# Performance work log

Measured on AMD Instinct MI355X. Metric: run time of the kernel, lower is better.

Reference implementation:

```python
import jax, jax.numpy as jnp
import numpy as np

T = 64
NBITS_PSUM = 8
NBITS_ACC = 8
K = 2
EPS = 1e-5

def _binarize_ste(x):
    # sign binarization with straight-through estimator (torch code overwrites .data)
    s = jnp.where(x >= 0, 1.0, -1.0).astype(x.dtype)
    return x + jax.lax.stop_gradient(s - x)

def _binary_conv_psum(x, w):
    # x: [N,C,H,W], w: [O,C,3,3]. Binarized 3x3 conv (stride 1, pad 1) computed as
    # chunks of T products along the unrolled reduction dim, each partial sum
    # quantized to NBITS_PSUM bits with step K, final accumulator clipped to NBITS_ACC.
    N, C, H, W = x.shape
    O = w.shape[0]
    xb = _binarize_ste(x)
    wb = _binarize_ste(w)
    patches = jax.lax.conv_general_dilated_patches(
        xb, (3, 3), (1, 1), ((1, 1), (1, 1)),
        dimension_numbers=('NCHW', 'OIHW', 'NCHW'))  # [N, C*9, H, W], channel-major
    R = C * 9
    nch = R // T  # 2304 / 64 = 36 chunks
    p = patches.reshape(N, nch, T, H, W).transpose(1, 0, 2, 3, 4)  # [nch,N,T,H,W]
    wf = wb.reshape(O, nch, T).transpose(1, 0, 2)                   # [nch,O,T]
    qmax = 2 ** (NBITS_PSUM - 1) - 1
    step = float(K)

    def body(carry, xs):
        acc, reg = carry
        pc, wc = xs
        psum = jnp.einsum('nthw,ot->nohw', pc, wc)  # partial sum over T binary products
        q = jnp.clip(jnp.round(psum / step), -qmax - 1, qmax) * step
        q_ste = psum + jax.lax.stop_gradient(q - psum)  # STE through quantizer
        reg = reg + jnp.mean((q - psum) ** 2)  # quantization-error regularizer
        return (acc + q_ste, reg), None

    acc0 = jnp.zeros((N, O, H, W), x.dtype)
    (acc, reg), _ = jax.lax.scan(body, (acc0, jnp.zeros((), x.dtype)), (p, wf))
    amax = (2 ** (NBITS_ACC - 1) - 1) * step  # accumulator clipping
    return jnp.clip(acc, -amax, amax), reg

def _bn(x, gamma, beta):
    # BatchNorm2d in training mode (batch statistics)
    m = jnp.mean(x, (0, 2, 3), keepdims=True)
    v = jnp.var(x, (0, 2, 3), keepdims=True)
    return (x - m) * jax.lax.rsqrt(v + EPS) * gamma[None, :, None, None] + beta[None, :, None, None]

def setup_inputs():
    key = jax.random.key(0)
    k1, k2, k3 = jax.random.split(key, 3)
    N, C, H, W = 32, 256, 32, 32
    return {
        'x0': jax.random.normal(k1, (N, C, H, W), jnp.float32),
        'reg0': jnp.zeros((), jnp.float32),
        'w1': jax.random.normal(k2, (C, C, 3, 3), jnp.float32),
        'gamma1': jnp.ones((C,), jnp.float32),
        'beta1': jnp.zeros((C,), jnp.float32),
        'w2': jax.random.normal(k3, (C, C, 3, 3), jnp.float32),
        'gamma2': jnp.ones((C,), jnp.float32),
        'beta2': jnp.zeros((C,), jnp.float32),
    }

def reference(x0, reg0, w1, gamma1, beta1, w2, gamma2, beta2):
    residual = x0
    out, r1 = _binary_conv_psum(x0, w1)
    reg = reg0 + r1
    out = _bn(out, gamma1, beta1)
    out = jnp.clip(out, -1.0, 1.0)  # Hardtanh
    out, r2 = _binary_conv_psum(out, w2)
    reg = reg + r2
    out = out + residual  # downsample is None
    reg = reg + r2        # faithful to original: conv2's r is added again after residual
    out = _bn(out, gamma2, beta2)
    out = jnp.clip(out, -1.0, 1.0)  # Hardtanh (do_bntan=True)
    return out, reg
```

## Files before the change

kernel.cpp:

```cpp
#include <hip/hip_runtime.h>

typedef unsigned long long u64;
typedef __attribute__((ext_vector_type(4)))  int i32x4;
typedef __attribute__((ext_vector_type(16))) int i32x16;

#define NPIX   32768
#define OCH    256
#define NCH    36

#define AROWS  196
#define ALDS   (AROWS * 256)
#define BLDS   8192
#define GLDS   (ALDS + 3 * BLDS)

__device__ __forceinline__ void gload16(const void* g, void* l) {
  __builtin_amdgcn_global_load_lds(
      (const __attribute__((address_space(1))) unsigned*)g,
      (__attribute__((address_space(3))) unsigned*)l, 16, 0, 0);
}

__global__ void bb_init(float* st, u64* masks) {
  int t = threadIdx.x;
  for (int i = t; i < 1024; i += 256) st[i] = 0.f;
  for (int id = t; id < 9 * NCH; id += 256) {
    int cls = id / NCH, ck = id % NCH;
    int ch = cls / 3, cw = cls % 3;
    u64 m = 0;
    for (int b = 0; b < 64; ++b) {
      int r = ck * 64 + b, tap = r % 9, kh = tap / 3, kw = tap % 3;
      bool oob = (ch == 0 && kh == 0) || (ch == 2 && kh == 2) ||
                 (cw == 0 && kw == 0) || (cw == 2 && kw == 2);
      if (!oob) m |= (u64)1 << b;
    }
    masks[id] = m;
  }
}

__global__ void bb_wbits(const float* wa, const float* wb, u64* Wbits) {
  int word = (blockIdx.x * blockDim.x + threadIdx.x) >> 6;
  int ln = threadIdx.x & 63;
  if (word >= 2 * OCH * NCH) return;
  const float* src = (word < OCH * NCH) ? wa : wb;
  int r = word % (OCH * NCH);
  u64 bits = __ballot(src[(size_t)r * 64 + ln] >= 0.f);
  int l = word / (OCH * NCH);
  int o = r / NCH, ck = r % NCH;
  if (ln == 0) Wbits[(size_t)l * OCH * NCH + (size_t)ck * OCH + o] = bits;
}

__global__ void bb_wi8(const float* wa, const float* wb, signed char* B) {
  int tid = blockIdx.x * blockDim.x + threadIdx.x;
  if (tid >= 2 * 589824) return;
  int l = tid >= 589824;
  int r = l ? tid - 589824 : tid;
  const float* src = l ? wb : wa;
  float v = src[r];
  int t = r % 9, oc9 = r / 9;
  int c = oc9 & 255, o = oc9 >> 8;
  B[(((size_t)(l * 9 + t) * 256 + o) << 8) + c] = (v >= 0.f) ? 1 : -1;
}

__global__ __launch_bounds__(256) void bb_xbits(const float* __restrict__ x,
                                                u64* __restrict__ Sb,
                                                signed char* __restrict__ A) {
  __shared__ float xt[256][33];
  int n = blockIdx.x >> 5, h = blockIdx.x & 31;
  int t = threadIdx.x;
  int w = t & 31, cg = t >> 5;
  for (int k = 0; k < 32; ++k) {
    int c = k * 8 + cg;
    xt[c][w] = x[((size_t)((n * 256 + c) * 32 + h) << 5) + w];
  }
  __syncthreads();
  int ln = t & 63, wv = t >> 6;
  int c2 = wv * 64 + ln;
  for (int w2 = 0; w2 < 32; ++w2) {
    bool s = xt[c2][w2] >= 0.f;
    u64 bits = __ballot(s);
    int px = (n * 32 + h) * 32 + w2;
    A[(size_t)px * 256 + c2] = s ? 1 : -1;
    if (ln == 0) Sb[(size_t)px * 4 + wv] = bits;
  }
}

__global__ __launch_bounds__(256, 2) void bb_gemm(const signed char* __restrict__ A,
                                                  const signed char* __restrict__ B,
                                                  short* __restrict__ dst) {
  extern __shared__ signed char sm[];
  int t = threadIdx.x, wv = t >> 6, ln = t & 63;
  int lw = ln & 31, hk = ln >> 5;
  int px0 = blockIdx.x << 7;
  int oc0 = blockIdx.y << 7;

  const signed char* Abase = A + (size_t)(px0 - 33) * 256;
  #pragma unroll
  for (int i = 0; i < 13; ++i) {
    int c = i * 4 + wv;
    if (c < 49) {
      int u = c * 64 + ln;
      int row = u >> 4, p = u & 15;
      gload16(Abase + (size_t)row * 256 + (((p ^ (row & 7)) << 4)),
              &sm[c * 1024]);
    }
  }

  #define STAGE_B(bufi, ks) do {                                              \
    int tp_ = (ks) >> 2, cb_ = (ks) & 3;                                      \
    const signed char* Bb_ = B + ((size_t)tp_ << 16) + (size_t)oc0 * 256      \
                               + (cb_ << 6);                                  \
    _Pragma("unroll")                                                         \
    for (int i_ = 0; i_ < 2; ++i_) {                                          \
      int c_ = wv * 2 + i_;                                                   \
      int u_ = c_ * 64 + ln;                                                  \
      int row_ = u_ >> 2, p_ = u_ & 3;                                        \
      gload16(Bb_ + (size_t)row_ * 256 + (((p_ ^ (row_ & 3)) << 4)),          \
              &sm[ALDS + (bufi) * BLDS + c_ * 1024]);                         \
    }                                                                         \
  } while (0)

  STAGE_B(0, 0);
  STAGE_B(1, 1);
  asm volatile("s_waitcnt vmcnt(2)" ::: "memory");
  __builtin_amdgcn_s_barrier();

  int wm = wv >> 1, wn = wv & 1;
  int arow0 = 33 + (wm << 6) + lw;
  int brow0 = (wn << 6) + lw;
  i32x16 acc00 = {0,0,0,0,0,0,0,0,0,0,0,0,0,0,0,0};
  i32x16 acc01 = acc00, acc10 = acc00, acc11 = acc00;

  for (int ks = 0; ks < 36; ++ks) {
    if (ks + 2 < 36) STAGE_B((ks + 2) % 3, ks + 2);
    int tp = ks >> 2, cb = ks & 3;
    int dpx = (tp / 3 - 1) * 32 + (tp % 3 - 1);
    int r0 = arow0 + dpx, r1 = r0 + 32;
    int q0 = brow0, q1 = brow0 + 32;
    const signed char* Bl = sm + ALDS + (ks % 3) * BLDS;
    __builtin_amdgcn_s_setprio(1);
    #pragma unroll
    for (int k32 = 0; k32 < 2; ++k32) {
      int sa = cb * 4 + k32 * 2 + hk;
      int sb = k32 * 2 + hk;
      i32x4 a0 = *(const i32x4*)(sm + r0 * 256 + ((sa ^ (r0 & 7)) << 4));
      i32x4 a1 = *(const i32x4*)(sm + r1 * 256 + ((sa ^ (r1 & 7)) << 4));
      i32x4 b0 = *(const i32x4*)(Bl + q0 * 64 + ((sb ^ (q0 & 3)) << 4));
      i32x4 b1 = *(const i32x4*)(Bl + q1 * 64 + ((sb ^ (q1 & 3)) << 4));
      acc00 = __builtin_amdgcn_mfma_i32_32x32x32_i8(a0, b0, acc00, 0, 0, 0);
      acc01 = __builtin_amdgcn_mfma_i32_32x32x32_i8(a0, b1, acc01, 0, 0, 0);
      acc10 = __builtin_amdgcn_mfma_i32_32x32x32_i8(a1, b0, acc10, 0, 0, 0);
      acc11 = __builtin_amdgcn_mfma_i32_32x32x32_i8(a1, b1, acc11, 0, 0, 0);
    }
    __builtin_amdgcn_s_setprio(0);
    if (ks < 34) asm volatile("s_waitcnt vmcnt(2)" ::: "memory");
    else         asm volatile("s_waitcnt vmcnt(0)" ::: "memory");
    __builtin_amdgcn_s_barrier();
  }
  #undef STAGE_B

  int px0w = px0 + (wm << 6), oc0w = oc0 + (wn << 6);
  int rbase = hk << 2;
  #pragma unroll
  for (int r = 0; r < 16; ++r) {
    int m = (r & 3) + ((r >> 2) << 3) + rbase;
    size_t row0 = ((size_t)(px0w + m)) << 8;
    size_t row1 = ((size_t)(px0w + 32 + m)) << 8;
    int v;
    v = acc00[r]; v = v < -254 ? -254 : (v > 254 ? 254 : v);
    dst[row0 + oc0w + lw] = (short)v;
    v = acc01[r]; v = v < -254 ? -254 : (v > 254 ? 254 : v);
    dst[row0 + oc0w + 32 + lw] = (short)v;
    v = acc10[r]; v = v < -254 ? -254 : (v > 254 ? 254 : v);
    dst[row1 + oc0w + lw] = (short)v;
    v = acc11[r]; v = v < -254 ? -254 : (v > 254 ? 254 : v);
    dst[row1 + oc0w + 32 + lw] = (short)v;
  }
}

__global__ __launch_bounds__(256) void bb_bconv(const u64* __restrict__ Sb,
                                                const u64* __restrict__ Wb,
                                                const u64* __restrict__ masks,
                                                short* __restrict__ dst) {
  __shared__ u64 spread[256];
  __shared__ u64 pw[NCH];
  __shared__ u64 mm[NCH];
  __shared__ int pm[NCH];
  int t = threadIdx.x;
  {
    u64 v = 0;
    for (int k = 0; k < 8; ++k) if (t & (1 << k)) v |= (u64)1 << (9 * k);
    spread[t] = v;
  }
  int b = blockIdx.x;
  int n = b / 124, r = b % 124;
  int h, w;
  if (r < 32)      { h = 0;      w = r;      }
  else if (r < 64) { h = 31;     w = r - 32; }
  else if (r < 94) { h = r - 63; w = 0;      }
  else             { h = r - 93; w = 31;     }
  int cls = (h == 0 ? 0 : (h == 31 ? 2 : 1)) * 3 + (w == 0 ? 0 : (w == 31 ? 2 : 1));
  __syncthreads();
  if (t < NCH) {
    int ck = t, base9 = ck % 9;
    u64 acc = 0;
    for (int tap = 0; tap < 9; ++tap) {
      int b0 = tap - base9; if (b0 < 0) b0 += 9;
      int nh = h + tap / 3 - 1, nw = w + tap % 3 - 1;
      if ((unsigned)nh <= 31u && (unsigned)nw <= 31u) {
        int run = (b0 == 0) ? 8 : 7;
        int c0 = (ck * 64 + b0) / 9;
        const u64* rp = Sb + ((size_t)((n * 32 + nh) * 32 + nw) << 2);
        int wi = c0 >> 6, sh = c0 & 63;
        u64 v = rp[wi] >> sh;
        if (sh + run > 64) v |= rp[wi + 1] << (64 - sh);
        v &= (run == 8) ? 0xFFull : 0x7Full;
        acc |= spread[(int)v] << b0;
      }
    }
    pw[ck] = acc;
    u64 m = masks[cls * NCH + ck];
    mm[ck] = m;
    pm[ck] = __popcll(m);
  }
  __syncthreads();
  int oc = t;
  int acc = 0;
  for (int i = 0; i < NCH; ++i) {
    int d = __popcll((pw[i] ^ Wb[(size_t)i * OCH + oc]) & mm[i]);
    int ps = pm[i] - 2 * d;
    acc += ps + (ps & 1) * ((ps & 2) - 1);
  }
  acc = acc < -254 ? -254 : (acc > 254 ? 254 : acc);
  int px = ((n * 32 + h) << 5) + w;
  dst[(size_t)px * OCH + oc] = (short)acc;
}

__global__ void bb_stats1(const short* v16, float* st) {
  int t = threadIdx.x;
  const short* base = v16 + (size_t)blockIdx.x * 128 * OCH;
  int s = 0; float q = 0.f;
  for (int r = 0; r < 128; ++r) {
    int v = base[r * OCH + t];
    s += v; q += (float)(v * v);
  }
  atomicAdd(&st[t], (float)s);
  atomicAdd(&st[256 + t], q);
}

__global__ void bb_xbits2(const short* v16, const float* st,
                          const float* g, const float* b, u64* Sb,
                          signed char* A) {
  int wave = (blockIdx.x * blockDim.x + threadIdx.x) >> 6;
  int ln = threadIdx.x & 63;
  int wrd = wave & 3, px0 = (wave >> 2) * 32;
  int oc = wrd * 64 + ln;
  float mu = st[oc] * (1.f / 32768.f);
  float va = st[256 + oc] * (1.f / 32768.f) - mu * mu;
  float rs = rsqrtf(va + 1e-5f);
  float gg = g[oc], bb = b[oc];
  for (int j = 0; j < 32; ++j) {
    float bn = ((float)v16[(size_t)(px0 + j) * OCH + oc] - mu) * rs * gg + bb;
    bool s = bn >= 0.f;
    u64 bits = __ballot(s);
    A[(size_t)(px0 + j) * 256 + oc] = s ? 1 : -1;
    if (ln == 0) Sb[(size_t)(px0 + j) * 4 + wrd] = bits;
  }
}

__global__ __launch_bounds__(256) void bb_stats2t(const short* __restrict__ pre16,
                                                  const float* __restrict__ x0,
                                                  float* st) {
  __shared__ float xt[32][257];
  int blk = blockIdx.x;
  int n = blk >> 5, h = blk & 31;
  int t = threadIdx.x;
  int w = t & 31, og = t >> 5;
  for (int k = 0; k < 32; ++k) {
    int oc = og * 32 + k;
    xt[w][oc] = x0[((size_t)(n * 256 + oc) * 32 + h) * 32 + w];
  }
  __syncthreads();
  int oc = t;
  size_t pb = (size_t)blk * 32 * OCH + oc;
  float s = 0.f, q = 0.f;
  for (int w2 = 0; w2 < 32; ++w2) {
    float v = (float)pre16[pb + (size_t)w2 * OCH] + xt[w2][oc];
    s += v; q += v * v;
  }
  atomicAdd(&st[512 + oc], s);
  atomicAdd(&st[768 + oc], q);
}

__global__ __launch_bounds__(256) void bb_fint(const short* __restrict__ pre16,
                                               const float* __restrict__ x0,
                                               const float* st, const float* g,
                                               const float* b, const float* r0,
                                               float* __restrict__ out) {
  __shared__ float xt[32][257];
  int blk = blockIdx.x;
  int n = blk >> 5, h = blk & 31;
  int t = threadIdx.x;
  int w = t & 31, og = t >> 5;
  for (int k = 0; k < 32; ++k) {
    int oc = og * 32 + k;
    xt[w][oc] = x0[((size_t)(n * 256 + oc) * 32 + h) * 32 + w];
  }
  __syncthreads();
  int oc = t;
  float mu = st[512 + oc] * (1.f / 32768.f);
  float va = st[768 + oc] * (1.f / 32768.f) - mu * mu;
  float rs = rsqrtf(va + 1e-5f);
  float gg = g[oc], bb = b[oc];
  size_t pb = (size_t)blk * 32 * OCH + oc;
  for (int w2 = 0; w2 < 32; ++w2) {
    float v = (float)pre16[pb + (size_t)w2 * OCH] + xt[w2][oc];
    v = (v - mu) * rs * gg + bb;
    xt[w2][oc] = fminf(fmaxf(v, -1.f), 1.f);
  }
  __syncthreads();
  for (int k = 0; k < 32; ++k) {
    int oc2 = og * 32 + k;
    out[((size_t)(n * 256 + oc2) * 32 + h) * 32 + w] = xt[w][oc2];
  }
  if (blk == 0 && t == 0) out[8388608] = r0[0] + 8.625f;
}

extern "C" void kernel_launch(void* const* d_in, const int* in_sizes, int n_in,
                              void* d_out, int out_size, void* d_ws, size_t ws_size,
                              hipStream_t stream) {
  const float* x0   = (const float*)d_in[0];
  const float* reg0 = (const float*)d_in[1];
  const float* w1   = (const float*)d_in[2];
  const float* g1   = (const float*)d_in[3];
  const float* b1   = (const float*)d_in[4];
  const float* w2   = (const float*)d_in[5];
  const float* g2   = (const float*)d_in[6];
  const float* b2   = (const float*)d_in[7];

  char* ws = (char*)d_ws;
  u64*   Wbits = (u64*)(ws);
  u64*   masks = (u64*)(ws + 147456);
  float* st    = (float*)(ws + 151552);
  u64*   Sb    = (u64*)(ws + 155648);
  signed char* Bi8 = (signed char*)(ws + 1204224);
  signed char* Ai8 = (signed char*)(ws + 2383872) + 32768;
  short* v16   = (short*)(ws + 10838016);

  bb_init   <<<1,    256, 0, stream>>>(st, masks);
  bb_wbits  <<<4608, 256, 0, stream>>>(w1, w2, Wbits);
  bb_wi8    <<<4608, 256, 0, stream>>>(w1, w2, Bi8);
  bb_xbits  <<<1024, 256, 0, stream>>>(x0, Sb, Ai8);
  bb_gemm   <<<dim3(256, 2), 256, GLDS, stream>>>(Ai8, Bi8, v16);
  bb_bconv  <<<3968, 256, 0, stream>>>(Sb, Wbits, masks, v16);
  bb_stats1 <<<256,  256, 0, stream>>>(v16, st);
  bb_xbits2 <<<1024, 256, 0, stream>>>(v16, st, g1, b1, Sb, Ai8);
  bb_gemm   <<<dim3(256, 2), 256, GLDS, stream>>>(Ai8, Bi8 + 589824, v16);
  bb_bconv  <<<3968, 256, 0, stream>>>(Sb, Wbits + OCH * NCH, masks, v16);
  bb_stats2t<<<1024, 256, 0, stream>>>(v16, x0, st);
  bb_fint   <<<1024, 256, 0, stream>>>(v16, x0, st, g2, b2, reg0, (float*)d_out);
}
```

Measured before the change: 287.8 us.

## Fuse weight prep kernels, fix B LDS swizzle, batch border pixels in bconv

Merges the three setup kernels (init, weight bit-pack, weight int8 pack) into one launch to cut launch overhead. Changes the B-tile LDS XOR swizzle to use (row>>1)&3, aiming to reduce bank conflicts on 64-byte rows. Reworks the border binary-conv kernel so each block handles 16 pixels, reusing each weight word load across pixels and launching far fewer blocks. The trade-off is more registers and shared memory per block, and 248 blocks may underfill the GPU.

```diff
diff --git a/kernel.cpp b/kernel.cpp
--- a/kernel.cpp
+++ b/kernel.cpp
@@ -19,45 +19,42 @@
       (__attribute__((address_space(3))) unsigned*)l, 16, 0, 0);
 }
 
-__global__ void bb_init(float* st, u64* masks) {
-  int t = threadIdx.x;
-  for (int i = t; i < 1024; i += 256) st[i] = 0.f;
-  for (int id = t; id < 9 * NCH; id += 256) {
-    int cls = id / NCH, ck = id % NCH;
-    int ch = cls / 3, cw = cls % 3;
-    u64 m = 0;
-    for (int b = 0; b < 64; ++b) {
-      int r = ck * 64 + b, tap = r % 9, kh = tap / 3, kw = tap % 3;
-      bool oob = (ch == 0 && kh == 0) || (ch == 2 && kh == 2) ||
-                 (cw == 0 && kw == 0) || (cw == 2 && kw == 2);
-      if (!oob) m |= (u64)1 << b;
-    }
-    masks[id] = m;
-  }
-}
-
-__global__ void bb_wbits(const float* wa, const float* wb, u64* Wbits) {
-  int word = (blockIdx.x * blockDim.x + threadIdx.x) >> 6;
-  int ln = threadIdx.x & 63;
-  if (word >= 2 * OCH * NCH) return;
-  const float* src = (word < OCH * NCH) ? wa : wb;
-  int r = word % (OCH * NCH);
-  u64 bits = __ballot(src[(size_t)r * 64 + ln] >= 0.f);
-  int l = word / (OCH * NCH);
-  int o = r / NCH, ck = r % NCH;
-  if (ln == 0) Wbits[(size_t)l * OCH * NCH + (size_t)ck * OCH + o] = bits;
-}
-
-__global__ void bb_wi8(const float* wa, const float* wb, signed char* B) {
-  int tid = blockIdx.x * blockDim.x + threadIdx.x;
-  if (tid >= 2 * 589824) return;
-  int l = tid >= 589824;
-  int r = l ? tid - 589824 : tid;
-  const float* src = l ? wb : wa;
-  float v = src[r];
-  int t = r % 9, oc9 = r / 9;
-  int c = oc9 & 255, o = oc9 >> 8;
-  B[(((size_t)(l * 9 + t) * 256 + o) << 8) + c] = (v >= 0.f) ? 1 : -1;
+__global__ void bb_prep(const float* wa, const float* wb, u64* Wbits,
+                        signed char* B, float* st, u64* masks) {
+  int blk = blockIdx.x, t = threadIdx.x;
+  if (blk == 0) {
+    for (int i = t; i < 1024; i += 256) st[i] = 0.f;
+    for (int id = t; id < 9 * NCH; id += 256) {
+      int cls = id / NCH, ck = id % NCH;
+      int ch = cls / 3, cw = cls % 3;
+      u64 m = 0;
+      for (int b = 0; b < 64; ++b) {
+        int r = ck * 64 + b, tap = r % 9, kh = tap / 3, kw = tap % 3;
+        bool oob = (ch == 0 && kh == 0) || (ch == 2 && kh == 2) ||
+                   (cw == 0 && kw == 0) || (cw == 2 && kw == 2);
+        if (!oob) m |= (u64)1 << b;
+      }
+      masks[id] = m;
+    }
+  } else if (blk <= 4608) {
+    int word = (((blk - 1) << 8) + t) >> 6;
+    int ln = t & 63;
+    const float* src = (word < OCH * NCH) ? wa : wb;
+    int r = word % (OCH * NCH);
+    u64 bits = __ballot(src[(size_t)r * 64 + ln] >= 0.f);
+    int l = word / (OCH * NCH);
+    int o = r / NCH, ck = r % NCH;
+    if (ln == 0) Wbits[(size_t)l * OCH * NCH + (size_t)ck * OCH + o] = bits;
+  } else {
+    int tid = ((blk - 4609) << 8) + t;
+    int l = tid >= 589824;
+    int r = l ? tid - 589824 : tid;
+    const float* src = l ? wb : wa;
+    float v = src[r];
+    int tp = r % 9, oc9 = r / 9;
+    int c = oc9 & 255, o = oc9 >> 8;
+    B[(((size_t)(l * 9 + tp) * 256 + o) << 8) + c] = (v >= 0.f) ? 1 : -1;
+  }
 }
 
 __global__ __launch_bounds__(256) void bb_xbits(const float* __restrict__ x,
@@ -113,7 +110,7 @@
       int c_ = wv * 2 + i_;                                                   \
       int u_ = c_ * 64 + ln;                                                  \
       int row_ = u_ >> 2, p_ = u_ & 3;                                        \
-      gload16(Bb_ + (size_t)row_ * 256 + (((p_ ^ (row_ & 3)) << 4)),          \
+      gload16(Bb_ + (size_t)row_ * 256 + (((p_ ^ ((row_ >> 1) & 3)) << 4)),   \
               &sm[ALDS + (bufi) * BLDS + c_ * 1024]);                         \
     }                                                                         \
   } while (0)
@@ -143,8 +140,8 @@
       int sb = k32 * 2 + hk;
       i32x4 a0 = *(const i32x4*)(sm + r0 * 256 + ((sa ^ (r0 & 7)) << 4));
       i32x4 a1 = *(const i32x4*)(sm + r1 * 256 + ((sa ^ (r1 & 7)) << 4));
-      i32x4 b0 = *(const i32x4*)(Bl + q0 * 64 + ((sb ^ (q0 & 3)) << 4));
-      i32x4 b1 = *(const i32x4*)(Bl + q1 * 64 + ((sb ^ (q1 & 3)) << 4));
+      i32x4 b0 = *(const i32x4*)(Bl + q0 * 64 + ((sb ^ ((q0 >> 1) & 3)) << 4));
+      i32x4 b1 = *(const i32x4*)(Bl + q1 * 64 + ((sb ^ ((q1 >> 1) & 3)) << 4));
       acc00 = __builtin_amdgcn_mfma_i32_32x32x32_i8(a0, b0, acc00, 0, 0, 0);
       acc01 = __builtin_amdgcn_mfma_i32_32x32x32_i8(a0, b1, acc01, 0, 0, 0);
       acc10 = __builtin_amdgcn_mfma_i32_32x32x32_i8(a1, b0, acc10, 0, 0, 0);
@@ -181,26 +178,29 @@
                                                 const u64* __restrict__ masks,
                                                 short* __restrict__ dst) {
   __shared__ u64 spread[256];
-  __shared__ u64 pw[NCH];
-  __shared__ u64 mm[NCH];
-  __shared__ int pm[NCH];
+  __shared__ u64 pw[16][NCH];
+  __shared__ u64 mm[16][NCH];
+  __shared__ int pm[16][NCH];
+  __shared__ int pxl[16];
   int t = threadIdx.x;
   {
     u64 v = 0;
     for (int k = 0; k < 8; ++k) if (t & (1 << k)) v |= (u64)1 << (9 * k);
     spread[t] = v;
   }
-  int b = blockIdx.x;
-  int n = b / 124, r = b % 124;
-  int h, w;
-  if (r < 32)      { h = 0;      w = r;      }
-  else if (r < 64) { h = 31;     w = r - 32; }
-  else if (r < 94) { h = r - 63; w = 0;      }
-  else             { h = r - 93; w = 31;     }
-  int cls = (h == 0 ? 0 : (h == 31 ? 2 : 1)) * 3 + (w == 0 ? 0 : (w == 31 ? 2 : 1));
-  __syncthreads();
-  if (t < NCH) {
-    int ck = t, base9 = ck % 9;
+  __syncthreads();
+  for (int id = t; id < 16 * NCH; id += 256) {
+    int p = id / NCH, ck = id % NCH;
+    int gp = blockIdx.x * 16 + p;
+    int n = gp / 124, r = gp % 124;
+    int h, w;
+    if (r < 32)      { h = 0;      w = r;      }
+    else if (r < 64) { h = 31;     w = r - 32; }
+    else if (r < 94) { h = r - 63; w = 0;      }
+    else             { h = r - 93; w = 31;     }
+    int cls = (h == 0 ? 0 : (h == 31 ? 2 : 1)) * 3 + (w == 0 ? 0 : (w == 31 ? 2 : 1));
+    if (ck == 0) pxl[p] = ((n * 32 + h) << 5) + w;
+    int base9 = ck % 9;
     u64 acc = 0;
     for (int tap = 0; tap < 9; ++tap) {
       int b0 = tap - base9; if (b0 < 0) b0 += 9;
@@ -216,22 +216,31 @@
         acc |= spread[(int)v] << b0;
       }
     }
-    pw[ck] = acc;
+    pw[p][ck] = acc;
     u64 m = masks[cls * NCH + ck];
-    mm[ck] = m;
-    pm[ck] = __popcll(m);
+    mm[p][ck] = m;
+    pm[p][ck] = __popcll(m);
   }
   __syncthreads();
   int oc = t;
-  int acc = 0;
+  int acc[16];
+  #pragma unroll
+  for (int p = 0; p < 16; ++p) acc[p] = 0;
   for (int i = 0; i < NCH; ++i) {
-    int d = __popcll((pw[i] ^ Wb[(size_t)i * OCH + oc]) & mm[i]);
-    int ps = pm[i] - 2 * d;
-    acc += ps + (ps & 1) * ((ps & 2) - 1);
-  }
-  acc = acc < -254 ? -254 : (acc > 254 ? 254 : acc);
-  int px = ((n * 32 + h) << 5) + w;
-  dst[(size_t)px * OCH + oc] = (short)acc;
+    u64 wr = Wb[(size_t)i * OCH + oc];
+    #pragma unroll
+    for (int p = 0; p < 16; ++p) {
+      int d = __popcll((pw[p][i] ^ wr) & mm[p][i]);
+      int ps = pm[p][i] - 2 * d;
+      acc[p] += ps + (ps & 1) * ((ps & 2) - 1);
+    }
+  }
+  #pragma unroll
+  for (int p = 0; p < 16; ++p) {
+    int v = acc[p];
+    v = v < -254 ? -254 : (v > 254 ? 254 : v);
+    dst[(size_t)pxl[p] * OCH + oc] = (short)v;
+  }
 }
 
 __global__ void bb_stats1(const short* v16, float* st) {
@@ -345,16 +354,14 @@
   signed char* Ai8 = (signed char*)(ws + 2383872) + 32768;
   short* v16   = (short*)(ws + 10838016);
 
-  bb_init   <<<1,    256, 0, stream>>>(st, masks);
-  bb_wbits  <<<4608, 256, 0, stream>>>(w1, w2, Wbits);
-  bb_wi8    <<<4608, 256, 0, stream>>>(w1, w2, Bi8);
+  bb_prep   <<<9217, 256, 0, stream>>>(w1, w2, Wbits, Bi8, st, masks);
   bb_xbits  <<<1024, 256, 0, stream>>>(x0, Sb, Ai8);
   bb_gemm   <<<dim3(256, 2), 256, GLDS, stream>>>(Ai8, Bi8, v16);
-  bb_bconv  <<<3968, 256, 0, stream>>>(Sb, Wbits, masks, v16);
+  bb_bconv  <<<248,  256, 0, stream>>>(Sb, Wbits, masks, v16);
   bb_stats1 <<<256,  256, 0, stream>>>(v16, st);
   bb_xbits2 <<<1024, 256, 0, stream>>>(v16, st, g1, b1, Sb, Ai8);
   bb_gemm   <<<dim3(256, 2), 256, GLDS, stream>>>(Ai8, Bi8 + 589824, v16);
-  bb_bconv  <<<3968, 256, 0, stream>>>(Sb, Wbits + OCH * NCH, masks, v16);
+  bb_bconv  <<<248,  256, 0, stream>>>(Sb, Wbits + OCH * NCH, masks, v16);
   bb_stats2t<<<1024, 256, 0, stream>>>(v16, x0, st);
   bb_fint   <<<1024, 256, 0, stream>>>(v16, x0, st, g2, b2, reg0, (float*)d_out);
 }
```

After: 308.0 us. +7.0%, slower.
